# Kernel tuning notes

Hardware: AMD Instinct MI355X
Metric: run time of the kernel (lower is better)

## Reference

```python
import math
import jax, jax.numpy as jnp
import numpy as np

B, S, D, H, DK = 2, 2048, 1024, 16, 64
NUM_BUCKETS, MAX_DISTANCE = 32, 128


def _relative_position_bucket(rel_pos):
    # bidirectional=True (encoder): is_decoder=False
    nb = NUM_BUCKETS // 2
    rel_buckets = (rel_pos > 0).astype(jnp.int32) * nb
    rp = jnp.abs(rel_pos)
    max_exact = nb // 2
    is_small = rp < max_exact
    rp_large = max_exact + (
        jnp.log(rp.astype(jnp.float32) / max_exact)
        / math.log(MAX_DISTANCE / max_exact)
        * (nb - max_exact)
    ).astype(jnp.int32)
    rp_large = jnp.minimum(rp_large, nb - 1)
    return rel_buckets + jnp.where(is_small, rp, rp_large)


def compute_bias(rel_bias, q_len, k_len):
    ctx = jnp.arange(q_len, dtype=jnp.int32)[:, None]
    mem = jnp.arange(k_len, dtype=jnp.int32)[None, :]
    buckets = _relative_position_bucket(mem - ctx)          # [q,k]
    vals = rel_bias[buckets]                                 # [q,k,H]
    return jnp.transpose(vals, (2, 0, 1))[None]              # [1,H,q,k]


def setup_inputs() -> dict:
    key = jax.random.key(0)
    ks = jax.random.split(key, 6)
    scale = 0.02
    return {
        "hidden_states": jax.random.normal(ks[0], (B, S, D), jnp.float32),
        "Wq": jax.random.normal(ks[1], (D, H * DK), jnp.float32) * scale,
        "Wk": jax.random.normal(ks[2], (D, H * DK), jnp.float32) * scale,
        "Wv": jax.random.normal(ks[3], (D, H * DK), jnp.float32) * scale,
        "Wo": jax.random.normal(ks[4], (H * DK, D), jnp.float32) * scale,
        "rel_bias": jax.random.normal(ks[5], (NUM_BUCKETS, H), jnp.float32) * scale,
    }


def reference(hidden_states, Wq, Wk, Wv, Wo, rel_bias):
    b, s, _ = hidden_states.shape

    def shape(x):  # [b,s,H*DK] -> [b,H,s,DK]
        return x.reshape(b, s, H, DK).transpose(0, 2, 1, 3)

    q = shape(hidden_states @ Wq)
    k = shape(hidden_states @ Wk)
    v = shape(hidden_states @ Wv)

    # T5: no 1/sqrt(d_k) scaling
    scores = jnp.einsum("bhqd,bhkd->bhqk", q, k)
    position_bias = compute_bias(rel_bias, s, s)             # [1,H,s,s]
    scores = scores + position_bias
    attn = jax.nn.softmax(scores.astype(jnp.float32), axis=-1).astype(scores.dtype)
    out = jnp.einsum("bhqk,bhkd->bhqd", attn, v)
    out = out.transpose(0, 2, 1, 3).reshape(b, s, H * DK)
    return out @ Wo
```

## Files before the change

kernel.cpp:

```cpp
#include <hip/hip_runtime.h>

#define HH 16
#define DKK 64
#define SS 2048
#define BB 2
#define DD 1024

typedef __attribute__((ext_vector_type(4))) float f32x4;
typedef __attribute__((ext_vector_type(8))) short bf16x8;
typedef __attribute__((ext_vector_type(4))) short s16x4;
typedef __attribute__((ext_vector_type(2))) int i32x2;

#define WAITCNT_VM0 0xF70

__device__ __forceinline__ short bf16b(float f) {
    union { float f; unsigned u; } x; x.f = f;
    unsigned r = (x.u + 0x7fffu + ((x.u >> 16) & 1u)) >> 16;
    return (short)r;
}

__device__ __forceinline__ unsigned f2u(float f) {
    union { float f; unsigned u; } x; x.f = f;
    return x.u;
}

__device__ __forceinline__ f32x4 mfma16(bf16x8 a, bf16x8 b, f32x4 c) {
    return __builtin_amdgcn_mfma_f32_16x16x32_bf16(a, b, c, 0, 0, 0);
}

__device__ __forceinline__ void lds16(const short* g, short* l) {
    __builtin_amdgcn_global_load_lds(
        (const __attribute__((address_space(1))) void*)g,
        (__attribute__((address_space(3))) void*)l, 16, 0, 0);
}

__global__ __launch_bounds__(256) void prep(
    const float* __restrict__ hs,
    const float* __restrict__ W0, const float* __restrict__ W1,
    const float* __restrict__ W2, const float* __restrict__ W3,
    const float* __restrict__ rb,
    short* __restrict__ hsb,
    short* __restrict__ T0, short* __restrict__ T1,
    short* __restrict__ T2, short* __restrict__ T3,
    float* __restrict__ tab) {
    __shared__ short tile[32][33];
    int blk = blockIdx.x, tid = threadIdx.x;
    if (blk < 4096) {
        int i = (blk * 256 + tid) * 4;
        f32x4 v = *(const f32x4*)(hs + i);
        s16x4 o;
        o.x = bf16b(v.x); o.y = bf16b(v.y); o.z = bf16b(v.z); o.w = bf16b(v.w);
        *(s16x4*)(hsb + i) = o;
    } else if (blk < 8192) {
        int t = blk - 4096;
        int z = t >> 10, r = t & 1023;
        int bx = r & 31, by = r >> 5;
        const float* W; short* T;
        switch (z) {
            case 0: W = W0; T = T0; break;
            case 1: W = W1; T = T1; break;
            case 2: W = W2; T = T2; break;
            default: W = W3; T = T3; break;
        }
        int n0 = bx * 32, k0 = by * 32;
        int tx = tid & 31, ty = (tid >> 5) * 4;
#pragma unroll
        for (int i = 0; i < 4; i++)
            tile[ty + i][tx] = bf16b(W[(k0 + ty + i) * DD + n0 + tx]);
        __syncthreads();
#pragma unroll
        for (int i = 0; i < 4; i++)
            T[(n0 + ty + i) * DD + k0 + tx] = tile[tx][ty + i];
    } else {
        int idx = (blk - 8192) * 256 + tid;
        if (idx < HH * 4095) {
            int h = idx / 4095, d = idx % 4095;
            int rel = d - 2047;
            int bucket = (rel > 0) ? 16 : 0;
            unsigned rr = (rel < 0) ? (unsigned)(-rel) : (unsigned)rel;
            int add;
            if (rr < 8) add = (int)rr;
            else {
                int e = 31 - __clz(rr);
                unsigned long long r2 = (unsigned long long)rr * (unsigned long long)rr;
                int f = 2 * e + ((r2 >= (2ull << (2 * e))) ? 1 : 0);
                add = 8 + (f - 6);
                if (add > 15) add = 15;
            }
            bucket += add;
            tab[h * 4095 + d] = rb[bucket * HH + h] * 1.44269504f;
        }
    }
}

__global__ __launch_bounds__(256) void gemm_qkv(
    const short* __restrict__ A, const short* __restrict__ Wt,
    short* __restrict__ Cq, short* __restrict__ Ck, short* __restrict__ Cvt) {
    const int K = 1024;
    __shared__ short As[128 * 32];
    __shared__ short Bs[128 * 32];
    int tid = threadIdx.x;
    int wave = tid >> 6, lane = tid & 63;
    int quad = lane >> 4, l16 = lane & 15;
    int m0 = blockIdx.y * 128, n0 = blockIdx.x * 128;

    int wm = (wave & 1) * 64, wn = (wave >> 1) * 64;
    int r0 = tid >> 2, c0 = (tid & 3) * 8;

    f32x4 acc[4][4];
#pragma unroll
    for (int i = 0; i < 4; i++)
#pragma unroll
        for (int j = 0; j < 4; j++) acc[i][j] = (f32x4){0.f, 0.f, 0.f, 0.f};

    for (int k0 = 0; k0 < K; k0 += 32) {
        __syncthreads();
        lds16(A + (size_t)(m0 + r0) * K + k0 + c0, As + wave * 512);
        lds16(A + (size_t)(m0 + 64 + r0) * K + k0 + c0, As + 2048 + wave * 512);
        lds16(Wt + (size_t)(n0 + r0) * K + k0 + c0, Bs + wave * 512);
        lds16(Wt + (size_t)(n0 + 64 + r0) * K + k0 + c0, Bs + 2048 + wave * 512);
        __syncthreads();
        bf16x8 af[4], bfr[4];
#pragma unroll
        for (int t = 0; t < 4; t++) {
            af[t] = *(const bf16x8*)(As + (wm + t * 16 + l16) * 32 + quad * 8);
            bfr[t] = *(const bf16x8*)(Bs + (wn + t * 16 + l16) * 32 + quad * 8);
        }
#pragma unroll
        for (int mt = 0; mt < 4; mt++)
#pragma unroll
            for (int nt = 0; nt < 4; nt++)
                acc[mt][nt] = mfma16(af[mt], bfr[nt], acc[mt][nt]);
    }

#pragma unroll
    for (int mt = 0; mt < 4; mt++) {
#pragma unroll
        for (int nt = 0; nt < 4; nt++) {
#pragma unroll
            for (int r = 0; r < 4; r++) {
                int gm = m0 + wm + mt * 16 + quad * 4 + r;
                int gn = n0 + wn + nt * 16 + l16;
                int b = gm >> 11, s = gm & 2047;
                int which = gn >> 10;
                int h = (gn >> 6) & 15, dk = gn & 63;
                short bv = bf16b(acc[mt][nt][r]);
                if (which == 0)
                    Cq[(((size_t)(b * HH + h)) * SS + s) * DKK + dk] = bv;
                else if (which == 1)
                    Ck[(((size_t)(b * HH + h)) * SS + s) * DKK + dk] = bv;
                else
                    Cvt[(((size_t)(b * HH + h)) * DKK + dk) * SS + s] = bv;
            }
        }
    }
}

__global__ __launch_bounds__(256) void gemm_out(
    const short* __restrict__ A, const short* __restrict__ Wt,
    float* __restrict__ Cout) {
    const int K = 1024, N = 1024;
    __shared__ short As[64 * 32];
    __shared__ short Bs[128 * 32];
    int tid = threadIdx.x;
    int wave = tid >> 6, lane = tid & 63;
    int quad = lane >> 4, l16 = lane & 15;
    int m0 = blockIdx.y * 64, n0 = blockIdx.x * 128;

    int wm = (wave & 1) * 32, wn = (wave >> 1) * 64;
    int r0 = tid >> 2, c0 = (tid & 3) * 8;

    f32x4 acc[2][4];
#pragma unroll
    for (int i = 0; i < 2; i++)
#pragma unroll
        for (int j = 0; j < 4; j++) acc[i][j] = (f32x4){0.f, 0.f, 0.f, 0.f};

    for (int k0 = 0; k0 < K; k0 += 32) {
        __syncthreads();
        lds16(A + (size_t)(m0 + r0) * K + k0 + c0, As + wave * 512);
        lds16(Wt + (size_t)(n0 + r0) * K + k0 + c0, Bs + wave * 512);
        lds16(Wt + (size_t)(n0 + 64 + r0) * K + k0 + c0, Bs + 2048 + wave * 512);
        __syncthreads();
        bf16x8 af[2], bfr[4];
#pragma unroll
        for (int t = 0; t < 2; t++)
            af[t] = *(const bf16x8*)(As + (wm + t * 16 + l16) * 32 + quad * 8);
#pragma unroll
        for (int t = 0; t < 4; t++)
            bfr[t] = *(const bf16x8*)(Bs + (wn + t * 16 + l16) * 32 + quad * 8);
#pragma unroll
        for (int mt = 0; mt < 2; mt++)
#pragma unroll
            for (int nt = 0; nt < 4; nt++)
                acc[mt][nt] = mfma16(af[mt], bfr[nt], acc[mt][nt]);
    }

#pragma unroll
    for (int mt = 0; mt < 2; mt++)
#pragma unroll
        for (int nt = 0; nt < 4; nt++)
#pragma unroll
            for (int r = 0; r < 4; r++) {
                int gm = m0 + wm + mt * 16 + quad * 4 + r;
                int gn = n0 + wn + nt * 16 + l16;
                Cout[(size_t)gm * N + gn] = acc[mt][nt][r];
            }
}

__global__ __launch_bounds__(256, 2) void attn(
    const short* __restrict__ Q, const short* __restrict__ Kmat,
    const short* __restrict__ Vt, const float* __restrict__ btab,
    short* __restrict__ O) {
    __shared__ short Ks[2][64 * 64];
    __shared__ short Vs[2][64 * 64];
    __shared__ float bias_s[2176];
    __shared__ short P_s[4][2][16 * 64];

    int tid = threadIdx.x;
    int wave = tid >> 6, lane = tid & 63;
    int quad = lane >> 4, l16 = lane & 15;
    int bh = blockIdx.x;
    int h = bh & 15, b = bh >> 4;
    int q0b = blockIdx.y * 128;
    int q0w = q0b + wave * 32;

    const short* Qb = Q + (size_t)bh * SS * DKK;
    const short* Kb = Kmat + (size_t)bh * SS * DKK;
    const short* Vb = Vt + (size_t)bh * DKK * SS;
    const float* bt = btab + h * 4095;

    int woff = 1920 - q0b;
    for (int i = tid; i < 2176; i += 256) {
        int gi = woff + i;
        bias_s[i] = bt[gi > 4094 ? 4094 : gi];
    }
    float blo = bt[2047 - 128];
    float bhi = bt[2047 + 128];

    int kro = tid >> 3;
    int gk = (tid & 7) ^ (kro & 7);
    const short* Kg0 = Kb + (size_t)kro * DKK + gk * 8;
    const short* Kg1 = Kb + (size_t)(kro + 32) * DKK + gk * 8;
    const short* Vg0 = Vb + (size_t)kro * SS + gk * 8;
    const short* Vg1 = Vb + (size_t)(kro + 32) * SS + gk * 8;

    bf16x8 qf[2][2];
#pragma unroll
    for (int qs = 0; qs < 2; qs++) {
        qf[qs][0] = *(const bf16x8*)(Qb + (q0w + qs * 16 + l16) * DKK + quad * 8);
        qf[qs][1] = *(const bf16x8*)(Qb + (q0w + qs * 16 + l16) * DKK + 32 + quad * 8);
    }

    f32x4 o[2][4];
#pragma unroll
    for (int qs = 0; qs < 2; qs++)
#pragma unroll
        for (int i = 0; i < 4; i++) o[qs][i] = (f32x4){0.f, 0.f, 0.f, 0.f};
    f32x4 lacc[2];
    lacc[0] = (f32x4){0.f, 0.f, 0.f, 0.f};
    lacc[1] = (f32x4){0.f, 0.f, 0.f, 0.f};

    bf16x8 onesf;
    short onev = (l16 == 0) ? (short)0x3F80 : (short)0;
#pragma unroll
    for (int i = 0; i < 8; i++) onesf[i] = onev;

    short* Pw = &P_s[wave][0][0];
    int gxor = l16 & 7;
    int ghalf = quad >> 1;
    int wbase = l16 * 64 + (quad & 1) * 4;
    int ra0 = l16 * 64 + ((quad ^ gxor) * 8);
    int ra1 = l16 * 64 + (((4 + quad) ^ gxor) * 8);
    int bidx = 127 + quad * 4 - wave * 32 - l16;
    int sl0 = (quad ^ gxor) * 8;
    int sl1 = ((4 + quad) ^ gxor) * 8;

    lds16(Kg0, &Ks[0][wave * 512]);
    lds16(Kg1, &Ks[0][2048 + wave * 512]);
    lds16(Vg0, &Vs[0][wave * 512]);
    lds16(Vg1, &Vs[0][2048 + wave * 512]);

    int cur = 0;
    for (int kc = 0; kc < SS; kc += 64) {
        __syncthreads();
        int kn = (kc + 64) & (SS - 1);
        int nxt = cur ^ 1;
        lds16(Kg0 + (size_t)kn * DKK, &Ks[nxt][wave * 512]);
        lds16(Kg1 + (size_t)kn * DKK, &Ks[nxt][2048 + wave * 512]);
        lds16(Vg0 + kn, &Vs[nxt][wave * 512]);
        lds16(Vg1 + kn, &Vs[nxt][2048 + wave * 512]);

        float breg[2][16];
#pragma unroll
        for (int qs = 0; qs < 2; qs++) {
            int q0s = q0w + qs * 16;
            if (kc > q0s - 191 && kc < q0s + 143) {
#pragma unroll
                for (int kt = 0; kt < 4; kt++)
#pragma unroll
                    for (int r = 0; r < 4; r++)
                        breg[qs][kt * 4 + r] =
                            bias_s[bidx + kc + kt * 16 + r - qs * 16];
            } else {
                float bc = (kc <= q0s - 191) ? blo : bhi;
#pragma unroll
                for (int i = 0; i < 16; i++) breg[qs][i] = bc;
            }
        }

        const short* Ksc = &Ks[cur][0];
        const short* Vsc = &Vs[cur][0];

        f32x4 s[2][4];
#pragma unroll
        for (int kt = 0; kt < 4; kt++) {
            int row = (kt * 16 + l16) * 64;
            bf16x8 kf0 = *(const bf16x8*)(Ksc + row + sl0);
            bf16x8 kf1 = *(const bf16x8*)(Ksc + row + sl1);
            s[0][kt] = mfma16(kf0, qf[0][0], (f32x4){0.f, 0.f, 0.f, 0.f});
            s[0][kt] = mfma16(kf1, qf[0][1], s[0][kt]);
            s[1][kt] = mfma16(kf0, qf[1][0], (f32x4){0.f, 0.f, 0.f, 0.f});
            s[1][kt] = mfma16(kf1, qf[1][1], s[1][kt]);
        }
        bf16x8 vf[4][2];
#pragma unroll
        for (int nt = 0; nt < 4; nt++) {
            int row = (nt * 16 + l16) * 64;
            vf[nt][0] = *(const bf16x8*)(Vsc + row + sl0);
            vf[nt][1] = *(const bf16x8*)(Vsc + row + sl1);
        }

#pragma unroll
        for (int qs = 0; qs < 2; qs++) {
#pragma unroll
            for (int kt = 0; kt < 4; kt++) {
                unsigned u[4];
#pragma unroll
                for (int r = 0; r < 4; r++) {
                    float p = __builtin_amdgcn_exp2f(
                        fmaf(s[qs][kt][r], 1.44269504f, breg[qs][kt * 4 + r]));
                    u[r] = f2u(p) + 0x8000u;
                }
                unsigned d0 = __builtin_amdgcn_perm(u[1], u[0], 0x07060302u);
                unsigned d1 = __builtin_amdgcn_perm(u[3], u[2], 0x07060302u);
                int g = (kt * 2 + ghalf) ^ gxor;
                *(i32x2*)(Pw + qs * 1024 + wbase + g * 8) = (i32x2){(int)d0, (int)d1};
            }
        }
        __asm__ __volatile__("" ::: "memory");
#pragma unroll
        for (int qs = 0; qs < 2; qs++) {
            bf16x8 pf0 = *(const bf16x8*)(Pw + qs * 1024 + ra0);
            bf16x8 pf1 = *(const bf16x8*)(Pw + qs * 1024 + ra1);
            lacc[qs] = mfma16(pf0, onesf, lacc[qs]);
            lacc[qs] = mfma16(pf1, onesf, lacc[qs]);
#pragma unroll
            for (int nt = 0; nt < 4; nt++) {
                o[qs][nt] = mfma16(pf0, vf[nt][0], o[qs][nt]);
                o[qs][nt] = mfma16(pf1, vf[nt][1], o[qs][nt]);
            }
        }
        __asm__ __volatile__("" ::: "memory");
        cur ^= 1;
    }
    __builtin_amdgcn_s_waitcnt(WAITCNT_VM0);

#pragma unroll
    for (int qs = 0; qs < 2; qs++) {
        float inv[4];
#pragma unroll
        for (int r = 0; r < 4; r++) {
            float l = __shfl(lacc[qs][r], lane & 48);
            inv[r] = 1.f / l;
        }
#pragma unroll
        for (int nt = 0; nt < 4; nt++)
#pragma unroll
            for (int r = 0; r < 4; r++) {
                int qrow = q0w + qs * 16 + quad * 4 + r;
                int dk = nt * 16 + l16;
                O[((size_t)(b * SS + qrow)) * (HH * DKK) + h * DKK + dk] =
                    bf16b(o[qs][nt][r] * inv[r]);
            }
    }
}

extern "C" void kernel_launch(void* const* d_in, const int* in_sizes, int n_in,
                              void* d_out, int out_size, void* d_ws, size_t ws_size,
                              hipStream_t stream) {
    const float* hs = (const float*)d_in[0];
    const float* Wq = (const float*)d_in[1];
    const float* Wk = (const float*)d_in[2];
    const float* Wv = (const float*)d_in[3];
    const float* Wo = (const float*)d_in[4];
    const float* rb = (const float*)d_in[5];
    float* out = (float*)d_out;

    char* ws = (char*)d_ws;
    size_t off = 0;
    auto alloc = [&](size_t bytes) -> void* {
        void* p = (void*)(ws + off);
        off += (bytes + 255) & ~(size_t)255;
        return p;
    };
    const size_t M = (size_t)BB * SS;
    short* hsb = (short*)alloc(M * DD * 2);
    short* WqT = (short*)alloc((size_t)DD * DD * 2);
    short* WkT = (short*)alloc((size_t)DD * DD * 2);
    short* WvT = (short*)alloc((size_t)DD * DD * 2);
    short* WoT = (short*)alloc((size_t)DD * DD * 2);
    short* Qb  = (short*)alloc(M * DD * 2);
    short* Kb  = (short*)alloc(M * DD * 2);
    short* VTb = (short*)alloc(M * DD * 2);
    short* Ab  = (short*)alloc(M * DD * 2);
    float* btab = (float*)alloc((size_t)HH * 4095 * 4);

    prep<<<8448, 256, 0, stream>>>(hs, Wq, Wk, Wv, Wo, rb,
                                   hsb, WqT, WkT, WvT, WoT, btab);
    gemm_qkv<<<dim3(24, 32), 256, 0, stream>>>(hsb, WqT, Qb, Kb, VTb);
    attn<<<dim3(32, 16), 256, 0, stream>>>(Qb, Kb, VTb, btab, Ab);
    gemm_out<<<dim3(8, 64), 256, 0, stream>>>(Ab, WoT, out);
}
```

Before: 193.4 us.

## Halve attention query tile per block, raise occupancy, read bias from global

The attention kernel now gives each wave 16 query rows instead of 32, so blocks cover 64 queries and the grid doubles to 32x32 blocks. Launch bounds are raised from 2 to 4 blocks per CU. The shared-memory bias window is removed, and the per-chunk bias values near the diagonal are loaded straight from the global bias table, which also shrinks the P staging buffer. The aim is more waves in flight and more blocks to fill the CUs. In exchange, each K/V tile staged in LDS is reused by half as many queries, doubling K/V global traffic, and the bias reads now go to global memory/cache.

```diff
diff --git a/kernel.cpp b/kernel.cpp
--- a/kernel.cpp
+++ b/kernel.cpp
@@ -208,33 +208,27 @@
             }
 }
 
-__global__ __launch_bounds__(256, 2) void attn(
+__global__ __launch_bounds__(256, 4) void attn(
     const short* __restrict__ Q, const short* __restrict__ Kmat,
     const short* __restrict__ Vt, const float* __restrict__ btab,
     short* __restrict__ O) {
     __shared__ short Ks[2][64 * 64];
     __shared__ short Vs[2][64 * 64];
-    __shared__ float bias_s[2176];
-    __shared__ short P_s[4][2][16 * 64];
+    __shared__ short P_s[4][16 * 64];
 
     int tid = threadIdx.x;
     int wave = tid >> 6, lane = tid & 63;
     int quad = lane >> 4, l16 = lane & 15;
     int bh = blockIdx.x;
     int h = bh & 15, b = bh >> 4;
-    int q0b = blockIdx.y * 128;
-    int q0w = q0b + wave * 32;
+    int q0b = blockIdx.y * 64;
+    int q0w = q0b + wave * 16;
 
     const short* Qb = Q + (size_t)bh * SS * DKK;
     const short* Kb = Kmat + (size_t)bh * SS * DKK;
     const short* Vb = Vt + (size_t)bh * DKK * SS;
     const float* bt = btab + h * 4095;
 
-    int woff = 1920 - q0b;
-    for (int i = tid; i < 2176; i += 256) {
-        int gi = woff + i;
-        bias_s[i] = bt[gi > 4094 ? 4094 : gi];
-    }
     float blo = bt[2047 - 128];
     float bhi = bt[2047 + 128];
 
@@ -245,36 +239,28 @@
     const short* Vg0 = Vb + (size_t)kro * SS + gk * 8;
     const short* Vg1 = Vb + (size_t)(kro + 32) * SS + gk * 8;
 
-    bf16x8 qf[2][2];
-#pragma unroll
-    for (int qs = 0; qs < 2; qs++) {
-        qf[qs][0] = *(const bf16x8*)(Qb + (q0w + qs * 16 + l16) * DKK + quad * 8);
-        qf[qs][1] = *(const bf16x8*)(Qb + (q0w + qs * 16 + l16) * DKK + 32 + quad * 8);
-    }
-
-    f32x4 o[2][4];
-#pragma unroll
-    for (int qs = 0; qs < 2; qs++)
-#pragma unroll
-        for (int i = 0; i < 4; i++) o[qs][i] = (f32x4){0.f, 0.f, 0.f, 0.f};
-    f32x4 lacc[2];
-    lacc[0] = (f32x4){0.f, 0.f, 0.f, 0.f};
-    lacc[1] = (f32x4){0.f, 0.f, 0.f, 0.f};
+    bf16x8 qf0 = *(const bf16x8*)(Qb + (q0w + l16) * DKK + quad * 8);
+    bf16x8 qf1 = *(const bf16x8*)(Qb + (q0w + l16) * DKK + 32 + quad * 8);
+
+    f32x4 o[4];
+#pragma unroll
+    for (int i = 0; i < 4; i++) o[i] = (f32x4){0.f, 0.f, 0.f, 0.f};
+    f32x4 lacc = (f32x4){0.f, 0.f, 0.f, 0.f};
 
     bf16x8 onesf;
     short onev = (l16 == 0) ? (short)0x3F80 : (short)0;
 #pragma unroll
     for (int i = 0; i < 8; i++) onesf[i] = onev;
 
-    short* Pw = &P_s[wave][0][0];
+    short* Pw = &P_s[wave][0];
     int gxor = l16 & 7;
     int ghalf = quad >> 1;
     int wbase = l16 * 64 + (quad & 1) * 4;
     int ra0 = l16 * 64 + ((quad ^ gxor) * 8);
     int ra1 = l16 * 64 + (((4 + quad) ^ gxor) * 8);
-    int bidx = 127 + quad * 4 - wave * 32 - l16;
     int sl0 = (quad ^ gxor) * 8;
     int sl1 = ((4 + quad) ^ gxor) * 8;
+    int bq = 2047 + quad * 4 - l16 - q0w;
 
     lds16(Kg0, &Ks[0][wave * 512]);
     lds16(Kg1, &Ks[0][2048 + wave * 512]);
@@ -291,37 +277,30 @@
         lds16(Vg0 + kn, &Vs[nxt][wave * 512]);
         lds16(Vg1 + kn, &Vs[nxt][2048 + wave * 512]);
 
-        float breg[2][16];
-#pragma unroll
-        for (int qs = 0; qs < 2; qs++) {
-            int q0s = q0w + qs * 16;
-            if (kc > q0s - 191 && kc < q0s + 143) {
-#pragma unroll
-                for (int kt = 0; kt < 4; kt++)
-#pragma unroll
-                    for (int r = 0; r < 4; r++)
-                        breg[qs][kt * 4 + r] =
-                            bias_s[bidx + kc + kt * 16 + r - qs * 16];
-            } else {
-                float bc = (kc <= q0s - 191) ? blo : bhi;
-#pragma unroll
-                for (int i = 0; i < 16; i++) breg[qs][i] = bc;
-            }
+        float breg[16];
+        if (kc > q0w - 191 && kc < q0w + 143) {
+#pragma unroll
+            for (int kt = 0; kt < 4; kt++)
+#pragma unroll
+                for (int r = 0; r < 4; r++)
+                    breg[kt * 4 + r] = bt[bq + kc + kt * 16 + r];
+        } else {
+            float bc = (kc <= q0w - 191) ? blo : bhi;
+#pragma unroll
+            for (int i = 0; i < 16; i++) breg[i] = bc;
         }
 
         const short* Ksc = &Ks[cur][0];
         const short* Vsc = &Vs[cur][0];
 
-        f32x4 s[2][4];
+        f32x4 s[4];
 #pragma unroll
         for (int kt = 0; kt < 4; kt++) {
             int row = (kt * 16 + l16) * 64;
             bf16x8 kf0 = *(const bf16x8*)(Ksc + row + sl0);
             bf16x8 kf1 = *(const bf16x8*)(Ksc + row + sl1);
-            s[0][kt] = mfma16(kf0, qf[0][0], (f32x4){0.f, 0.f, 0.f, 0.f});
-            s[0][kt] = mfma16(kf1, qf[0][1], s[0][kt]);
-            s[1][kt] = mfma16(kf0, qf[1][0], (f32x4){0.f, 0.f, 0.f, 0.f});
-            s[1][kt] = mfma16(kf1, qf[1][1], s[1][kt]);
+            s[kt] = mfma16(kf0, qf0, (f32x4){0.f, 0.f, 0.f, 0.f});
+            s[kt] = mfma16(kf1, qf1, s[kt]);
         }
         bf16x8 vf[4][2];
 #pragma unroll
@@ -332,33 +311,29 @@
         }
 
 #pragma unroll
-        for (int qs = 0; qs < 2; qs++) {
-#pragma unroll
-            for (int kt = 0; kt < 4; kt++) {
-                unsigned u[4];
-#pragma unroll
-                for (int r = 0; r < 4; r++) {
-                    float p = __builtin_amdgcn_exp2f(
-                        fmaf(s[qs][kt][r], 1.44269504f, breg[qs][kt * 4 + r]));
-                    u[r] = f2u(p) + 0x8000u;
-                }
-                unsigned d0 = __builtin_amdgcn_perm(u[1], u[0], 0x07060302u);
-                unsigned d1 = __builtin_amdgcn_perm(u[3], u[2], 0x07060302u);
-                int g = (kt * 2 + ghalf) ^ gxor;
-                *(i32x2*)(Pw + qs * 1024 + wbase + g * 8) = (i32x2){(int)d0, (int)d1};
-            }
+        for (int kt = 0; kt < 4; kt++) {
+            unsigned u[4];
+#pragma unroll
+            for (int r = 0; r < 4; r++) {
+                float p = __builtin_amdgcn_exp2f(
+                    fmaf(s[kt][r], 1.44269504f, breg[kt * 4 + r]));
+                u[r] = f2u(p) + 0x8000u;
+            }
+            unsigned d0 = __builtin_amdgcn_perm(u[1], u[0], 0x07060302u);
+            unsigned d1 = __builtin_amdgcn_perm(u[3], u[2], 0x07060302u);
+            int g = (kt * 2 + ghalf) ^ gxor;
+            *(i32x2*)(Pw + wbase + g * 8) = (i32x2){(int)d0, (int)d1};
         }
         __asm__ __volatile__("" ::: "memory");
-#pragma unroll
-        for (int qs = 0; qs < 2; qs++) {
-            bf16x8 pf0 = *(const bf16x8*)(Pw + qs * 1024 + ra0);
-            bf16x8 pf1 = *(const bf16x8*)(Pw + qs * 1024 + ra1);
-            lacc[qs] = mfma16(pf0, onesf, lacc[qs]);
-            lacc[qs] = mfma16(pf1, onesf, lacc[qs]);
+        {
+            bf16x8 pf0 = *(const bf16x8*)(Pw + ra0);
+            bf16x8 pf1 = *(const bf16x8*)(Pw + ra1);
+            lacc = mfma16(pf0, onesf, lacc);
+            lacc = mfma16(pf1, onesf, lacc);
 #pragma unroll
             for (int nt = 0; nt < 4; nt++) {
-                o[qs][nt] = mfma16(pf0, vf[nt][0], o[qs][nt]);
-                o[qs][nt] = mfma16(pf1, vf[nt][1], o[qs][nt]);
+                o[nt] = mfma16(pf0, vf[nt][0], o[nt]);
+                o[nt] = mfma16(pf1, vf[nt][1], o[nt]);
             }
         }
         __asm__ __volatile__("" ::: "memory");
@@ -366,24 +341,21 @@
     }
     __builtin_amdgcn_s_waitcnt(WAITCNT_VM0);
 
-#pragma unroll
-    for (int qs = 0; qs < 2; qs++) {
-        float inv[4];
+    float inv[4];
+#pragma unroll
+    for (int r = 0; r < 4; r++) {
+        float l = __shfl(lacc[r], lane & 48);
+        inv[r] = 1.f / l;
+    }
+#pragma unroll
+    for (int nt = 0; nt < 4; nt++)
 #pragma unroll
         for (int r = 0; r < 4; r++) {
-            float l = __shfl(lacc[qs][r], lane & 48);
-            inv[r] = 1.f / l;
-        }
-#pragma unroll
-        for (int nt = 0; nt < 4; nt++)
-#pragma unroll
-            for (int r = 0; r < 4; r++) {
-                int qrow = q0w + qs * 16 + quad * 4 + r;
-                int dk = nt * 16 + l16;
-                O[((size_t)(b * SS + qrow)) * (HH * DKK) + h * DKK + dk] =
-                    bf16b(o[qs][nt][r] * inv[r]);
-            }
-    }
+            int qrow = q0w + quad * 4 + r;
+            int dk = nt * 16 + l16;
+            O[((size_t)(b * SS + qrow)) * (HH * DKK) + h * DKK + dk] =
+                bf16b(o[nt][r] * inv[r]);
+        }
 }
 
 extern "C" void kernel_launch(void* const* d_in, const int* in_sizes, int n_in,
@@ -419,6 +391,6 @@
     prep<<<8448, 256, 0, stream>>>(hs, Wq, Wk, Wv, Wo, rb,
                                    hsb, WqT, WkT, WvT, WoT, btab);
     gemm_qkv<<<dim3(24, 32), 256, 0, stream>>>(hsb, WqT, Qb, Kb, VTb);
-    attn<<<dim3(32, 16), 256, 0, stream>>>(Qb, Kb, VTb, btab, Ab);
+    attn<<<dim3(32, 32), 256, 0, stream>>>(Qb, Kb, VTb, btab, Ab);
     gemm_out<<<dim3(8, 64), 256, 0, stream>>>(Ab, WoT, out);
 }
```

After: 196.5 us. About the same (+1.6%).
